# Kernel optimization log

Measured on AMD Instinct MI355X. Metric: run time of the kernel, lower is better.

The kernel has to match this reference:

```python
import jax, jax.numpy as jnp
from jax import lax
import numpy as np

B, N = 8, 16384
C = 16            # layer_channels
K = 2             # kernel_size
L = 30            # layer_nums (layer 0 is plain causal conv, 29 gated layers)
AGG = 64          # agregate1x1 out channels
OUT = 256         # output1x1 out channels (8-bit classes)


def causal_conv(x, w, dilation):
    # x: (B, Cin, N), w: (Cout, Cin, K) -> (B, Cout, N), left-padded (causal)
    k = w.shape[-1]
    return lax.conv_general_dilated(
        x, w, window_strides=(1,), padding=[(dilation * (k - 1), 0)],
        rhs_dilation=(dilation,), dimension_numbers=('NCH', 'OIH', 'NCH'))


def setup_inputs() -> dict:
    key = jax.random.key(0)
    ks = jax.random.split(key, 16)
    s = 0.1
    x = jax.random.normal(ks[0], (B, N), dtype=jnp.float32) * 8000.0  # raw 16-bit-ish audio
    lengths = jax.random.randint(ks[1], (B,), N // 2, N, dtype=jnp.int32)
    return {
        'x': x,
        'lengths': lengths,
        'W0': jax.random.normal(ks[2], (C, 1, K), dtype=jnp.float32) * s,
        'b0': jnp.zeros((C,), dtype=jnp.float32),
        'Wf': jax.random.normal(ks[3], (L - 1, C, C, K), dtype=jnp.float32) * s,
        'bf': jnp.zeros((L - 1, C), dtype=jnp.float32),
        'Wg': jax.random.normal(ks[4], (L - 1, C, C, K), dtype=jnp.float32) * s,
        'bg': jnp.zeros((L - 1, C), dtype=jnp.float32),
        'Wr': jax.random.normal(ks[5], (L - 1, C, C), dtype=jnp.float32) * s,
        'br': jnp.zeros((L - 1, C), dtype=jnp.float32),
        'Wa': jax.random.normal(ks[6], (AGG, C), dtype=jnp.float32) * s,
        'ba': jnp.zeros((AGG,), dtype=jnp.float32),
        'Wo': jax.random.normal(ks[7], (OUT, AGG), dtype=jnp.float32) * s,
        'bo': jnp.zeros((OUT,), dtype=jnp.float32),
    }


def reference(x, lengths, W0, b0, Wf, bf, Wg, bg, Wr, br, Wa, ba, Wo, bo):
    inp = (x / 32768.0)[:, None, :]                     # (B,1,N), 65536/2 scaling
    # layer 0: plain causal conv 1 -> C
    h = causal_conv(inp, W0, 1) + b0[:, None]           # (B,C,N)
    skip = h
    inp = inp + h                                       # (B,1,N)+(B,C,N) broadcast
    for i in range(1, L):
        d = 2 ** (i % 10)
        j = i - 1
        f = jnp.tanh(causal_conv(inp, Wf[j], d) + bf[j][:, None])
        g = jax.nn.sigmoid(causal_conv(inp, Wg[j], d) + bg[j][:, None])
        z = f * g                                       # gated activation
        out = jnp.einsum('oc,bcn->bon', Wr[j], z) + br[j][:, None]
        skip = skip + out                               # skip-sum accumulation
        inp = inp + out                                 # residual
    a = jnp.einsum('oc,bcn->bon', Wa, jax.nn.relu(skip)) + ba[:, None]
    o = jnp.einsum('oc,bcn->bon', Wo, jax.nn.relu(a)) + bo[:, None]
    logp = jax.nn.log_softmax(o, axis=1)                # (B,OUT,N)
    mask = (jnp.arange(N) < lengths[:, None])[:, None, :].astype(logp.dtype)
    return logp * mask
```

## Files before the change

### kernel.cpp

```cpp
#include <hip/hip_runtime.h>
#include <hip/hip_bf16.h>

#define NN 16384
#define NC 16
#define NPOSTOT 131072
#define NLAY 29
#define TOUT 256
#define LSTR 24

typedef float4 f4;
typedef short bf16x8 __attribute__((ext_vector_type(8)));
typedef float f32x4 __attribute__((ext_vector_type(4)));

#define OFF_WF 0
#define OFF_WG (NLAY * 512)
#define OFF_WR (2 * NLAY * 512)
#define OFF_WA (3 * NLAY * 512)
#define OFF_WO (3 * NLAY * 512 + 2048)
#define PK_TOT (OFF_WO + 16384)

static __device__ __forceinline__ short to_bf16(float f) {
    __hip_bfloat16 h = __float2bfloat16(f);
    short s;
    __builtin_memcpy(&s, &h, 2);
    return s;
}
static __device__ __forceinline__ float from_bf16(short s) {
    unsigned int u = ((unsigned int)(unsigned short)s) << 16;
    float f;
    __builtin_memcpy(&f, &u, 4);
    return f;
}

__global__ __launch_bounds__(256) void prepack_k(
    const float* __restrict__ Wf, const float* __restrict__ Wg,
    const float* __restrict__ Wr, const float* __restrict__ Wa,
    const float* __restrict__ Wo, short* __restrict__ pk)
{
    const int i = blockIdx.x * 256 + threadIdx.x;
    if (i >= PK_TOT) return;
    float val;
    if (i < OFF_WG) {
        const int j = i >> 9, r = i & 511, l = r >> 3, j8 = r & 7;
        const int o = l & 15, h = l >> 4;
        const int k = h * 8 + j8, tap = k >> 4, c = k & 15;
        val = Wf[((j * 16 + o) * 16 + c) * 2 + tap];
    } else if (i < OFF_WA) {
        const int i2 = i - OFF_WG;
        if (i2 < NLAY * 512) {
            const int j = i2 >> 9, r = i2 & 511, l = r >> 3, j8 = r & 7;
            const int o = l & 15, h = l >> 4;
            const int k = h * 8 + j8, tap = k >> 4, c = k & 15;
            val = Wg[((j * 16 + o) * 16 + c) * 2 + tap];
        } else {
            const int i3 = i2 - NLAY * 512;
            const int j = i3 >> 9, r = i3 & 511, l = r >> 3, j8 = r & 7;
            const int o = l & 15, h = l >> 4;
            val = (j8 < 4) ? Wr[j * 256 + o * 16 + h * 4 + j8] : 0.0f;
        }
    } else if (i < OFF_WO) {
        const int i2 = i - OFF_WA;
        const int mt = i2 >> 9, r = i2 & 511, l = r >> 3, j8 = r & 7;
        const int og = mt * 16 + (l & 15), h = l >> 4;
        const int k = h * 8 + j8;
        val = (k < 16) ? Wa[og * 16 + k] : 0.0f;
    } else {
        const int i2 = i - OFF_WO;
        const int qt = i2 >> 10, hf = (i2 >> 9) & 1, r = i2 & 511;
        const int l = r >> 3, j8 = r & 7;
        const int q = qt * 16 + (l & 15), h = l >> 4;
        const int kg = hf * 32 + (j8 >> 2) * 16 + h * 4 + (j8 & 3);
        val = Wo[q * 64 + kg];
    }
    pk[i] = to_bf16(val);
}

static __device__ __forceinline__ f32x4 gated_core2(
    bf16x8 bx, bf16x8 af_, bf16x8 ag_, bf16x8 ar_,
    f32x4 cf, f32x4 cg, f32x4 cr)
{
    const f32x4 fp = __builtin_amdgcn_mfma_f32_16x16x32_bf16(af_, bx, cf, 0, 0, 0);
    const f32x4 gp = __builtin_amdgcn_mfma_f32_16x16x32_bf16(ag_, bx, cg, 0, 0, 0);

    bf16x8 bz;
#pragma unroll
    for (int r = 0; r < 4; ++r) {
        const float ef = __expf(2.0f * fminf(fp[r], 43.0f));
        const float eg = __expf(-gp[r]);
        const float den = fmaf(ef, eg, ef) + (eg + 1.0f);
        bz[r] = to_bf16((ef - 1.0f) * __builtin_amdgcn_rcpf(den));
        bz[r + 4] = 0;
    }
    return __builtin_amdgcn_mfma_f32_16x16x32_bf16(ar_, bz, cr, 0, 0, 0);
}

struct SegCfg { int d[8]; int nl; int jbase; int H; int l0; };

__global__ __launch_bounds__(1024) void fused_k(
    const short* __restrict__ src, const float* __restrict__ x,
    const float* __restrict__ W0, const float* __restrict__ b0,
    short* __restrict__ dst, const short* __restrict__ pk,
    const float* __restrict__ bfA, const float* __restrict__ bgA,
    const float* __restrict__ brA, SegCfg cfg)
{
    extern __shared__ short lds[];
    const int H = cfg.H;
    const int Wp = TOUT + H;
    short* ldsA = lds;
    short* ldsB = lds + Wp * LSTR;

    const int t = threadIdx.x, lane = t & 63, wv = t >> 6;
    const int h = lane >> 4, i16 = lane & 15;
    const int tap = h >> 1, c0 = (h & 1) * 8;
    const int pbase = blockIdx.x * TOUT;
    const int bb = pbase >> 14, n0 = pbase & (NN - 1);
    const float* xrow = x + (size_t)bb * NN;
    const short* srow = src + (size_t)bb * NN * NC;

    const int l0r = wv * 32 + i16;
    const int l1r = l0r + 16;
    const int nA = n0 - H + l0r;
    const int nB = nA + 16;

    f32x4 res0, res1;

    {
        const int d = cfg.d[0];
        const int j = cfg.jbase;
        const bf16x8 af = *(const bf16x8*)(pk + OFF_WF + j * 512 + lane * 8);
        const bf16x8 ag = *(const bf16x8*)(pk + OFF_WG + j * 512 + lane * 8);
        const bf16x8 ar = *(const bf16x8*)(pk + OFF_WR + j * 512 + lane * 8);
        const f4 v1 = *(const f4*)(bfA + j * 16 + h * 4);
        const f4 v2 = *(const f4*)(bgA + j * 16 + h * 4);
        const f4 v3 = *(const f4*)(brA + j * 16 + h * 4);
        const f32x4 cf = {v1.x, v1.y, v1.z, v1.w};
        const f32x4 cg = {v2.x, v2.y, v2.z, v2.w};
        const f32x4 cr = {v3.x, v3.y, v3.z, v3.w};

        auto tile0 = [&](int l, int n, f32x4& res) {
            const int ns = tap ? n : n - d;
            bf16x8 bx = {0, 0, 0, 0, 0, 0, 0, 0};
            if (cfg.l0) {
                if (ns >= 0) {
                    const float xs = xrow[ns] * (1.0f / 32768.0f);
                    const float xm = (ns >= 1) ? xrow[ns - 1] * (1.0f / 32768.0f) : 0.0f;
#pragma unroll
                    for (int q2 = 0; q2 < 8; ++q2) {
                        const int c = c0 + q2;
                        bx[q2] = to_bf16(xs + fmaf(W0[c * 2], xm,
                                          fmaf(W0[c * 2 + 1], xs, b0[c])));
                    }
                }
            } else {
                if (ns >= 0) bx = *(const bf16x8*)(srow + (size_t)ns * NC + c0);
            }
            const f32x4 o = gated_core2(bx, af, ag, ar, cf, cg, cr);

            float r0, r1, r2, r3;
            if (cfg.l0) {
                if (n >= 0) {
                    const float xs = xrow[n] * (1.0f / 32768.0f);
                    const float xm = (n >= 1) ? xrow[n - 1] * (1.0f / 32768.0f) : 0.0f;
                    const int c = h * 4;
                    r0 = xs + fmaf(W0[c * 2 + 0], xm, fmaf(W0[c * 2 + 1], xs, b0[c + 0]));
                    r1 = xs + fmaf(W0[c * 2 + 2], xm, fmaf(W0[c * 2 + 3], xs, b0[c + 1]));
                    r2 = xs + fmaf(W0[c * 2 + 4], xm, fmaf(W0[c * 2 + 5], xs, b0[c + 2]));
                    r3 = xs + fmaf(W0[c * 2 + 6], xm, fmaf(W0[c * 2 + 7], xs, b0[c + 3]));
                } else { r0 = r1 = r2 = r3 = 0.0f; }
            } else {
                if (n >= 0) {
                    const short4 ov = *(const short4*)(srow + (size_t)n * NC + h * 4);
                    r0 = from_bf16(ov.x); r1 = from_bf16(ov.y);
                    r2 = from_bf16(ov.z); r3 = from_bf16(ov.w);
                } else { r0 = r1 = r2 = r3 = 0.0f; }
            }
            res[0] = r0 + o[0]; res[1] = r1 + o[1];
            res[2] = r2 + o[2]; res[3] = r3 + o[3];
            *(short4*)(ldsA + l * LSTR + h * 4) =
                make_short4(to_bf16(res[0]), to_bf16(res[1]),
                            to_bf16(res[2]), to_bf16(res[3]));
        };
        tile0(l0r, nA, res0);
        tile0(l1r, nB, res1);
    }
    __syncthreads();

    int cur = 0;
    for (int s = 1; s < cfg.nl; ++s) {
        const int d = cfg.d[s];
        const int j = cfg.jbase + s;
        const bf16x8 af = *(const bf16x8*)(pk + OFF_WF + j * 512 + lane * 8);
        const bf16x8 ag = *(const bf16x8*)(pk + OFF_WG + j * 512 + lane * 8);
        const bf16x8 ar = *(const bf16x8*)(pk + OFF_WR + j * 512 + lane * 8);
        const f4 v1 = *(const f4*)(bfA + j * 16 + h * 4);
        const f4 v2 = *(const f4*)(bgA + j * 16 + h * 4);
        const f4 v3 = *(const f4*)(brA + j * 16 + h * 4);
        const f32x4 cf = {v1.x, v1.y, v1.z, v1.w};
        const f32x4 cg = {v2.x, v2.y, v2.z, v2.w};
        const f32x4 cr = {v3.x, v3.y, v3.z, v3.w};
        const short* rb = cur ? ldsB : ldsA;
        short* wb = cur ? ldsA : ldsB;

        auto tileL = [&](int l, int n, f32x4& res) {
            const int nt = tap ? n : n - d;
            int lt = tap ? l : l - d;
            if (lt < 0) lt = 0;
            bf16x8 bx = {0, 0, 0, 0, 0, 0, 0, 0};
            if (nt >= 0) bx = *(const bf16x8*)(rb + lt * LSTR + c0);
            const f32x4 o = gated_core2(bx, af, ag, ar, cf, cg, cr);
            res[0] += o[0]; res[1] += o[1]; res[2] += o[2]; res[3] += o[3];
            *(short4*)(wb + l * LSTR + h * 4) =
                make_short4(to_bf16(res[0]), to_bf16(res[1]),
                            to_bf16(res[2]), to_bf16(res[3]));
        };
        tileL(l0r, nA, res0);
        tileL(l1r, nB, res1);
        __syncthreads();
        cur ^= 1;
    }

    if (l0r >= H) {
        *(short4*)(dst + ((size_t)bb * NN + nA) * NC + h * 4) =
            make_short4(to_bf16(res0[0]), to_bf16(res0[1]),
                        to_bf16(res0[2]), to_bf16(res0[3]));
    }
    if (l1r >= H) {
        *(short4*)(dst + ((size_t)bb * NN + nB) * NC + h * 4) =
            make_short4(to_bf16(res1[0]), to_bf16(res1[1]),
                        to_bf16(res1[2]), to_bf16(res1[3]));
    }
}

__global__ __launch_bounds__(256) void headm_k(
    const short* __restrict__ fin, const float* __restrict__ x,
    const int* __restrict__ lengths,
    const short* __restrict__ pka, const float* __restrict__ ba,
    const short* __restrict__ pko, const float* __restrict__ bo,
    float* __restrict__ out)
{
    const int t = threadIdx.x;
    const int lane = t & 63;
    const int wv = t >> 6;
    const int pos = blockIdx.x * 64 + wv * 16 + (lane & 15);
    const int h = lane >> 4;
    const int b = pos >> 14;
    const int n = pos & (NN - 1);

    bf16x8 bs;
    if (h < 2) {
        const float xs = x[pos] * (1.0f / 32768.0f);
        const bf16x8 v = *(const bf16x8*)(fin + (size_t)pos * NC + h * 8);
#pragma unroll
        for (int j = 0; j < 8; ++j)
            bs[j] = to_bf16(fmaxf(from_bf16(v[j]) - xs, 0.0f));
    } else {
#pragma unroll
        for (int j = 0; j < 8; ++j) bs[j] = 0;
    }

    float ra[16];
#pragma unroll
    for (int mt = 0; mt < 4; ++mt) {
        const bf16x8 aa = *(const bf16x8*)(pka + (mt * 64 + lane) * 8);
        const f4 bav = *(const f4*)(ba + mt * 16 + h * 4);
        f32x4 c = {bav.x, bav.y, bav.z, bav.w};
        c = __builtin_amdgcn_mfma_f32_16x16x32_bf16(aa, bs, c, 0, 0, 0);
#pragma unroll
        for (int r = 0; r < 4; ++r) ra[mt * 4 + r] = fmaxf(c[r], 0.0f);
    }
    bf16x8 blo, bhi;
#pragma unroll
    for (int j = 0; j < 8; ++j) { blo[j] = to_bf16(ra[j]); bhi[j] = to_bf16(ra[8 + j]); }

    float lg[64];
#pragma unroll
    for (int qt = 0; qt < 16; ++qt) {
        const bf16x8 a0 = *(const bf16x8*)(pko + ((qt * 2 + 0) * 64 + lane) * 8);
        const bf16x8 a1 = *(const bf16x8*)(pko + ((qt * 2 + 1) * 64 + lane) * 8);
        const f4 bov = *(const f4*)(bo + qt * 16 + h * 4);
        f32x4 c = {bov.x, bov.y, bov.z, bov.w};
        c = __builtin_amdgcn_mfma_f32_16x16x32_bf16(a0, blo, c, 0, 0, 0);
        c = __builtin_amdgcn_mfma_f32_16x16x32_bf16(a1, bhi, c, 0, 0, 0);
#pragma unroll
        for (int r = 0; r < 4; ++r) lg[qt * 4 + r] = c[r];
    }

    float m = lg[0];
#pragma unroll
    for (int j = 1; j < 64; ++j) m = fmaxf(m, lg[j]);
    m = fmaxf(m, __shfl_xor(m, 16, 64));
    m = fmaxf(m, __shfl_xor(m, 32, 64));
    float s = 0.0f;
#pragma unroll
    for (int j = 0; j < 64; ++j) s += __expf(lg[j] - m);
    s += __shfl_xor(s, 16, 64);
    s += __shfl_xor(s, 32, 64);
    const float lse = m + __logf(s);
    const bool valid = n < lengths[b];

    float* ob = out + (size_t)b * 256 * NN + n;
#pragma unroll
    for (int qt = 0; qt < 16; ++qt)
#pragma unroll
        for (int r = 0; r < 4; ++r)
            ob[(size_t)(qt * 16 + h * 4 + r) * NN] = valid ? (lg[qt * 4 + r] - lse) : 0.0f;
}

extern "C" void kernel_launch(void* const* d_in, const int* in_sizes, int n_in,
                              void* d_out, int out_size, void* d_ws, size_t ws_size,
                              hipStream_t stream)
{
    const float* x       = (const float*)d_in[0];
    const int*   lengths = (const int*)d_in[1];
    const float* W0      = (const float*)d_in[2];
    const float* b0      = (const float*)d_in[3];
    const float* Wf      = (const float*)d_in[4];
    const float* bf      = (const float*)d_in[5];
    const float* Wg      = (const float*)d_in[6];
    const float* bg      = (const float*)d_in[7];
    const float* Wr      = (const float*)d_in[8];
    const float* br      = (const float*)d_in[9];
    const float* Wa      = (const float*)d_in[10];
    const float* ba      = (const float*)d_in[11];
    const float* Wo      = (const float*)d_in[12];
    const float* bo      = (const float*)d_in[13];
    float* out = (float*)d_out;

    short* bufA = (short*)d_ws;
    short* bufB = bufA + (size_t)NPOSTOT * NC;
    short* pk   = bufB + (size_t)NPOSTOT * NC;

    prepack_k<<<dim3((PK_TOT + 255) / 256), dim3(256), 0, stream>>>(
        Wf, Wg, Wr, Wa, Wo, pk);

    const SegCfg cfgs[9] = {
        {{2, 4, 8, 16, 32, 64, 0, 0},  6, 0,  128, 1},
        {{128, 256, 0, 0, 0, 0, 0, 0}, 2, 6,  256, 0},
        {{512, 1, 2, 4, 8, 16, 32, 0}, 7, 8,  64,  0},
        {{64, 128, 0, 0, 0, 0, 0, 0},  2, 15, 128, 0},
        {{256, 0, 0, 0, 0, 0, 0, 0},   1, 17, 0,   0},
        {{512, 1, 2, 4, 8, 16, 32, 0}, 7, 18, 64,  0},
        {{64, 128, 0, 0, 0, 0, 0, 0},  2, 25, 128, 0},
        {{256, 0, 0, 0, 0, 0, 0, 0},   1, 27, 0,   0},
        {{512, 0, 0, 0, 0, 0, 0, 0},   1, 28, 0,   0},
    };

    const short* cursrc = bufA;
    short* bufs[2] = {bufA, bufB};
    int cur = 0;
    for (int k = 0; k < 9; ++k) {
        const SegCfg& c = cfgs[k];
        const int Wp = TOUT + c.H;
        const dim3 blk(Wp * 2);
        const size_t sh = (size_t)2 * Wp * LSTR * sizeof(short);
        short* d = bufs[cur];
        fused_k<<<dim3(NPOSTOT / TOUT), blk, sh, stream>>>(
            cursrc, x, W0, b0, d, pk, bf, bg, br, c);
        cursrc = d;
        cur ^= 1;
    }

    headm_k<<<dim3(NPOSTOT / 64), dim3(256), 0, stream>>>(
        bufA, x, lengths, pk + OFF_WA, ba, pk + OFF_WO, bo, out);
}
```

Before: 151.1 us.

## Use fixed 512-thread blocks with multi-tile waves, prefetch weights, and coalesce head stores

The fused gated-layer kernel now launches a fixed 512-thread block, with each wave looping over up to four 16-row tiles, in place of a block size that scaled with the halo. The next layer's weight fragments are prefetched while the current layer computes. A lighter LDS barrier replaces __syncthreads, and LDS writes and shared memory are skipped for single-layer segments. The head kernel stages log-softmax outputs through a shared-memory transpose so each wave writes contiguous 64-float rows instead of strided scalar stores, at the cost of extra LDS traffic and block barriers.

```diff
diff --git a/kernel.cpp b/kernel.cpp
--- a/kernel.cpp
+++ b/kernel.cpp
@@ -7,6 +7,7 @@
 #define NLAY 29
 #define TOUT 256
 #define LSTR 24
+#define MAXT 4
 
 typedef float4 f4;
 typedef short bf16x8 __attribute__((ext_vector_type(8)));
@@ -94,9 +95,28 @@
     return __builtin_amdgcn_mfma_f32_16x16x32_bf16(ar_, bz, cr, 0, 0, 0);
 }
 
+#define LDFRAG(J, AF, AG, AR, CF, CG, CR) do {                            \
+    AF = *(const bf16x8*)(pk + OFF_WF + (J) * 512 + lane * 8);            \
+    AG = *(const bf16x8*)(pk + OFF_WG + (J) * 512 + lane * 8);            \
+    AR = *(const bf16x8*)(pk + OFF_WR + (J) * 512 + lane * 8);            \
+    const f4 v1_ = *(const f4*)(bfA + (J) * 16 + h * 4);                  \
+    const f4 v2_ = *(const f4*)(bgA + (J) * 16 + h * 4);                  \
+    const f4 v3_ = *(const f4*)(brA + (J) * 16 + h * 4);                  \
+    CF[0] = v1_.x; CF[1] = v1_.y; CF[2] = v1_.z; CF[3] = v1_.w;           \
+    CG[0] = v2_.x; CG[1] = v2_.y; CG[2] = v2_.z; CG[3] = v2_.w;           \
+    CR[0] = v3_.x; CR[1] = v3_.y; CR[2] = v3_.z; CR[3] = v3_.w;           \
+} while (0)
+
+static __device__ __forceinline__ void lds_barrier() {
+    asm volatile("s_waitcnt lgkmcnt(0)" ::: "memory");
+    __builtin_amdgcn_sched_barrier(0);
+    __builtin_amdgcn_s_barrier();
+    __builtin_amdgcn_sched_barrier(0);
+}
+
 struct SegCfg { int d[8]; int nl; int jbase; int H; int l0; };
 
-__global__ __launch_bounds__(1024) void fused_k(
+__global__ __launch_bounds__(512, 4) void fused_k(
     const short* __restrict__ src, const float* __restrict__ x,
     const float* __restrict__ W0, const float* __restrict__ b0,
     short* __restrict__ dst, const short* __restrict__ pk,
@@ -106,6 +126,7 @@
     extern __shared__ short lds[];
     const int H = cfg.H;
     const int Wp = TOUT + H;
+    const int ntile = Wp >> 4;
     short* ldsA = lds;
     short* ldsB = lds + Wp * LSTR;
 
@@ -117,29 +138,26 @@
     const float* xrow = x + (size_t)bb * NN;
     const short* srow = src + (size_t)bb * NN * NC;
 
-    const int l0r = wv * 32 + i16;
-    const int l1r = l0r + 16;
-    const int nA = n0 - H + l0r;
-    const int nB = nA + 16;
-
-    f32x4 res0, res1;
+    f32x4 res[MAXT];
+
+    bf16x8 afC, agC, arC, afN, agN, arN;
+    f32x4 cfC, cgC, crC, cfN, cgN, crN;
+    LDFRAG(cfg.jbase, afC, agC, arC, cfC, cgC, crC);
+    if (cfg.nl > 1) LDFRAG(cfg.jbase + 1, afN, agN, arN, cfN, cgN, crN);
 
     {
         const int d = cfg.d[0];
-        const int j = cfg.jbase;
-        const bf16x8 af = *(const bf16x8*)(pk + OFF_WF + j * 512 + lane * 8);
-        const bf16x8 ag = *(const bf16x8*)(pk + OFF_WG + j * 512 + lane * 8);
-        const bf16x8 ar = *(const bf16x8*)(pk + OFF_WR + j * 512 + lane * 8);
-        const f4 v1 = *(const f4*)(bfA + j * 16 + h * 4);
-        const f4 v2 = *(const f4*)(bgA + j * 16 + h * 4);
-        const f4 v3 = *(const f4*)(brA + j * 16 + h * 4);
-        const f32x4 cf = {v1.x, v1.y, v1.z, v1.w};
-        const f32x4 cg = {v2.x, v2.y, v2.z, v2.w};
-        const f32x4 cr = {v3.x, v3.y, v3.z, v3.w};
-
-        auto tile0 = [&](int l, int n, f32x4& res) {
+        bf16x8 bx[MAXT];
+        f32x4 rin[MAXT];
+#pragma unroll
+        for (int k = 0; k < MAXT; ++k) {
+            const int tile = wv + 8 * k;
+            if (tile >= ntile) continue;
+            const int l = tile * 16 + i16;
+            const int n = n0 - H + l;
             const int ns = tap ? n : n - d;
-            bf16x8 bx = {0, 0, 0, 0, 0, 0, 0, 0};
+            bf16x8 b = {0, 0, 0, 0, 0, 0, 0, 0};
+            f32x4 r = {0.0f, 0.0f, 0.0f, 0.0f};
             if (cfg.l0) {
                 if (ns >= 0) {
                     const float xs = xrow[ns] * (1.0f / 32768.0f);
@@ -147,87 +165,94 @@
 #pragma unroll
                     for (int q2 = 0; q2 < 8; ++q2) {
                         const int c = c0 + q2;
-                        bx[q2] = to_bf16(xs + fmaf(W0[c * 2], xm,
-                                          fmaf(W0[c * 2 + 1], xs, b0[c])));
+                        b[q2] = to_bf16(xs + fmaf(W0[c * 2], xm,
+                                         fmaf(W0[c * 2 + 1], xs, b0[c])));
                     }
                 }
-            } else {
-                if (ns >= 0) bx = *(const bf16x8*)(srow + (size_t)ns * NC + c0);
-            }
-            const f32x4 o = gated_core2(bx, af, ag, ar, cf, cg, cr);
-
-            float r0, r1, r2, r3;
-            if (cfg.l0) {
                 if (n >= 0) {
                     const float xs = xrow[n] * (1.0f / 32768.0f);
                     const float xm = (n >= 1) ? xrow[n - 1] * (1.0f / 32768.0f) : 0.0f;
                     const int c = h * 4;
-                    r0 = xs + fmaf(W0[c * 2 + 0], xm, fmaf(W0[c * 2 + 1], xs, b0[c + 0]));
-                    r1 = xs + fmaf(W0[c * 2 + 2], xm, fmaf(W0[c * 2 + 3], xs, b0[c + 1]));
-                    r2 = xs + fmaf(W0[c * 2 + 4], xm, fmaf(W0[c * 2 + 5], xs, b0[c + 2]));
-                    r3 = xs + fmaf(W0[c * 2 + 6], xm, fmaf(W0[c * 2 + 7], xs, b0[c + 3]));
-                } else { r0 = r1 = r2 = r3 = 0.0f; }
+                    r[0] = xs + fmaf(W0[c * 2 + 0], xm, fmaf(W0[c * 2 + 1], xs, b0[c + 0]));
+                    r[1] = xs + fmaf(W0[c * 2 + 2], xm, fmaf(W0[c * 2 + 3], xs, b0[c + 1]));
+                    r[2] = xs + fmaf(W0[c * 2 + 4], xm, fmaf(W0[c * 2 + 5], xs, b0[c + 2]));
+                    r[3] = xs + fmaf(W0[c * 2 + 6], xm, fmaf(W0[c * 2 + 7], xs, b0[c + 3]));
+                }
             } else {
+                if (ns >= 0) b = *(const bf16x8*)(srow + (size_t)ns * NC + c0);
                 if (n >= 0) {
                     const short4 ov = *(const short4*)(srow + (size_t)n * NC + h * 4);
-                    r0 = from_bf16(ov.x); r1 = from_bf16(ov.y);
-                    r2 = from_bf16(ov.z); r3 = from_bf16(ov.w);
-                } else { r0 = r1 = r2 = r3 = 0.0f; }
+                    r[0] = from_bf16(ov.x); r[1] = from_bf16(ov.y);
+                    r[2] = from_bf16(ov.z); r[3] = from_bf16(ov.w);
+                }
             }
-            res[0] = r0 + o[0]; res[1] = r1 + o[1];
-            res[2] = r2 + o[2]; res[3] = r3 + o[3];
-            *(short4*)(ldsA + l * LSTR + h * 4) =
-                make_short4(to_bf16(res[0]), to_bf16(res[1]),
-                            to_bf16(res[2]), to_bf16(res[3]));
-        };
-        tile0(l0r, nA, res0);
-        tile0(l1r, nB, res1);
-    }
-    __syncthreads();
+            bx[k] = b;
+            rin[k] = r;
+        }
+#pragma unroll
+        for (int k = 0; k < MAXT; ++k) {
+            const int tile = wv + 8 * k;
+            if (tile >= ntile) continue;
+            const f32x4 o = gated_core2(bx[k], afC, agC, arC, cfC, cgC, crC);
+            res[k] = rin[k] + o;
+            if (cfg.nl > 1) {
+                const int l = tile * 16 + i16;
+                *(short4*)(ldsA + l * LSTR + h * 4) =
+                    make_short4(to_bf16(res[k][0]), to_bf16(res[k][1]),
+                                to_bf16(res[k][2]), to_bf16(res[k][3]));
+            }
+        }
+    }
 
     int cur = 0;
     for (int s = 1; s < cfg.nl; ++s) {
+        afC = afN; agC = agN; arC = arN; cfC = cfN; cgC = cgN; crC = crN;
+        if (s + 1 < cfg.nl) LDFRAG(cfg.jbase + s + 1, afN, agN, arN, cfN, cgN, crN);
         const int d = cfg.d[s];
-        const int j = cfg.jbase + s;
-        const bf16x8 af = *(const bf16x8*)(pk + OFF_WF + j * 512 + lane * 8);
-        const bf16x8 ag = *(const bf16x8*)(pk + OFF_WG + j * 512 + lane * 8);
-        const bf16x8 ar = *(const bf16x8*)(pk + OFF_WR + j * 512 + lane * 8);
-        const f4 v1 = *(const f4*)(bfA + j * 16 + h * 4);
-        const f4 v2 = *(const f4*)(bgA + j * 16 + h * 4);
-        const f4 v3 = *(const f4*)(brA + j * 16 + h * 4);
-        const f32x4 cf = {v1.x, v1.y, v1.z, v1.w};
-        const f32x4 cg = {v2.x, v2.y, v2.z, v2.w};
-        const f32x4 cr = {v3.x, v3.y, v3.z, v3.w};
+        lds_barrier();
         const short* rb = cur ? ldsB : ldsA;
         short* wb = cur ? ldsA : ldsB;
-
-        auto tileL = [&](int l, int n, f32x4& res) {
+        const bool wr = (s + 1 < cfg.nl);
+
+        bf16x8 bx[MAXT];
+#pragma unroll
+        for (int k = 0; k < MAXT; ++k) {
+            const int tile = wv + 8 * k;
+            if (tile >= ntile) continue;
+            const int l = tile * 16 + i16;
+            const int n = n0 - H + l;
             const int nt = tap ? n : n - d;
             int lt = tap ? l : l - d;
             if (lt < 0) lt = 0;
-            bf16x8 bx = {0, 0, 0, 0, 0, 0, 0, 0};
-            if (nt >= 0) bx = *(const bf16x8*)(rb + lt * LSTR + c0);
-            const f32x4 o = gated_core2(bx, af, ag, ar, cf, cg, cr);
-            res[0] += o[0]; res[1] += o[1]; res[2] += o[2]; res[3] += o[3];
-            *(short4*)(wb + l * LSTR + h * 4) =
-                make_short4(to_bf16(res[0]), to_bf16(res[1]),
-                            to_bf16(res[2]), to_bf16(res[3]));
-        };
-        tileL(l0r, nA, res0);
-        tileL(l1r, nB, res1);
-        __syncthreads();
+            bf16x8 b = {0, 0, 0, 0, 0, 0, 0, 0};
+            if (nt >= 0) b = *(const bf16x8*)(rb + lt * LSTR + c0);
+            bx[k] = b;
+        }
+#pragma unroll
+        for (int k = 0; k < MAXT; ++k) {
+            const int tile = wv + 8 * k;
+            if (tile >= ntile) continue;
+            const f32x4 o = gated_core2(bx[k], afC, agC, arC, cfC, cgC, crC);
+            res[k] += o;
+            if (wr) {
+                const int l = tile * 16 + i16;
+                *(short4*)(wb + l * LSTR + h * 4) =
+                    make_short4(to_bf16(res[k][0]), to_bf16(res[k][1]),
+                                to_bf16(res[k][2]), to_bf16(res[k][3]));
+            }
+        }
         cur ^= 1;
     }
 
-    if (l0r >= H) {
-        *(short4*)(dst + ((size_t)bb * NN + nA) * NC + h * 4) =
-            make_short4(to_bf16(res0[0]), to_bf16(res0[1]),
-                        to_bf16(res0[2]), to_bf16(res0[3]));
-    }
-    if (l1r >= H) {
-        *(short4*)(dst + ((size_t)bb * NN + nB) * NC + h * 4) =
-            make_short4(to_bf16(res1[0]), to_bf16(res1[1]),
-                        to_bf16(res1[2]), to_bf16(res1[3]));
+#pragma unroll
+    for (int k = 0; k < MAXT; ++k) {
+        const int tile = wv + 8 * k;
+        if (tile >= ntile || tile < (H >> 4)) continue;
+        const int l = tile * 16 + i16;
+        const int n = n0 - H + l;
+        *(short4*)(dst + ((size_t)bb * NN + n) * NC + h * 4) =
+            make_short4(to_bf16(res[k][0]), to_bf16(res[k][1]),
+                        to_bf16(res[k][2]), to_bf16(res[k][3]));
     }
 }
 
@@ -238,13 +263,17 @@
     const short* __restrict__ pko, const float* __restrict__ bo,
     float* __restrict__ out)
 {
+    __shared__ float lt_[64][68];
+
     const int t = threadIdx.x;
     const int lane = t & 63;
     const int wv = t >> 6;
-    const int pos = blockIdx.x * 64 + wv * 16 + (lane & 15);
+    const int i16 = lane & 15;
     const int h = lane >> 4;
+    const int pos = blockIdx.x * 64 + wv * 16 + i16;
     const int b = pos >> 14;
     const int n = pos & (NN - 1);
+    const int nblk = (blockIdx.x * 64) & (NN - 1);
 
     bf16x8 bs;
     if (h < 2) {
@@ -297,13 +326,25 @@
     s += __shfl_xor(s, 32, 64);
     const float lse = m + __logf(s);
     const bool valid = n < lengths[b];
-
-    float* ob = out + (size_t)b * 256 * NN + n;
-#pragma unroll
-    for (int qt = 0; qt < 16; ++qt)
-#pragma unroll
-        for (int r = 0; r < 4; ++r)
-            ob[(size_t)(qt * 16 + h * 4 + r) * NN] = valid ? (lg[qt * 4 + r] - lse) : 0.0f;
+#pragma unroll
+    for (int j = 0; j < 64; ++j) lg[j] = valid ? (lg[j] - lse) : 0.0f;
+
+    float* ob = out + (size_t)b * 256 * NN + nblk;
+#pragma unroll 1
+    for (int c = 0; c < 4; ++c) {
+#pragma unroll
+        for (int qq = 0; qq < 4; ++qq)
+#pragma unroll
+            for (int r = 0; r < 4; ++r)
+                lt_[qq * 16 + h * 4 + r][wv * 16 + i16] = lg[(c * 4 + qq) * 4 + r];
+        __syncthreads();
+#pragma unroll
+        for (int u = 0; u < 16; ++u) {
+            const int q = c * 64 + wv * 16 + u;
+            ob[(size_t)q * NN + lane] = lt_[wv * 16 + u][lane];
+        }
+        __syncthreads();
+    }
 }
 
 extern "C" void kernel_launch(void* const* d_in, const int* in_sizes, int n_in,
@@ -351,10 +392,9 @@
     for (int k = 0; k < 9; ++k) {
         const SegCfg& c = cfgs[k];
         const int Wp = TOUT + c.H;
-        const dim3 blk(Wp * 2);
-        const size_t sh = (size_t)2 * Wp * LSTR * sizeof(short);
+        const size_t sh = (c.nl > 1) ? (size_t)2 * Wp * LSTR * sizeof(short) : 0;
         short* d = bufs[cur];
-        fused_k<<<dim3(NPOSTOT / TOUT), blk, sh, stream>>>(
+        fused_k<<<dim3(NPOSTOT / TOUT), dim3(512), sh, stream>>>(
             cursrc, x, W0, b0, d, pk, bf, bg, br, c);
         cursrc = d;
         cur ^= 1;
```

New measurement: 196.2 us. +29.8%, slower.
